# Kernel tuning notes

Hardware: AMD Instinct MI355X
Metric: run time of the kernel (lower is better)

The kernel has to match this reference:

```python
import jax, jax.numpy as jnp
import numpy as np

EMBED_DIM = 1024
HEAD_DIM = 64


def setup_inputs() -> dict:
    key = jax.random.key(0)
    k1, k2, k3, k4 = jax.random.split(key, 4)
    B, T = 4, 4096
    x = jax.random.normal(k1, (B, T, EMBED_DIM), dtype=jnp.float32)
    # nn.Linear(EMBED_DIM, head_dim, bias=False): store as (EMBED_DIM, head_dim)
    s = (1.0 / np.sqrt(EMBED_DIM)).astype(np.float32)
    Wk = jax.random.uniform(k2, (EMBED_DIM, HEAD_DIM), jnp.float32, -s, s)
    Wq = jax.random.uniform(k3, (EMBED_DIM, HEAD_DIM), jnp.float32, -s, s)
    Wv = jax.random.uniform(k4, (EMBED_DIM, HEAD_DIM), jnp.float32, -s, s)
    return {"x": x, "Wq": Wq, "Wk": Wk, "Wv": Wv}


def reference(x, Wq, Wk, Wv):
    B, T, E = x.shape
    q = jnp.einsum('bte,ed->btd', x, Wq)  # (B,T,D)
    k = jnp.einsum('bte,ed->btd', x, Wk)
    v = jnp.einsum('bte,ed->btd', x, Wv)
    # NOTE: original scales by EMBED_DIM**-0.5 (x.size(-1)), not head_dim**-0.5
    scale = jnp.asarray(E, x.dtype) ** -0.5
    scores = jnp.einsum('bqd,bkd->bqk', q, k) * scale  # (B,T,T)
    causal = jnp.tril(jnp.ones((T, T), dtype=bool))
    scores = jnp.where(causal, scores, jnp.asarray(-jnp.inf, scores.dtype))
    attn = jax.nn.softmax(scores, axis=-1)
    # dropout is identity at inference (deterministic baseline)
    out = jnp.einsum('bqk,bkd->bqd', attn, v)  # (B,T,D)
    return out
```

## Files before the change

### kernel.cpp

```cpp
#include <hip/hip_runtime.h>
#include <hip/hip_bf16.h>
#include <stdint.h>

#define BATCH 4
#define SEQ   4096
#define EMB   1024
#define HD    64

typedef __bf16 bf16x8 __attribute__((ext_vector_type(8)));
typedef float  f32x4  __attribute__((ext_vector_type(4)));
typedef unsigned short u16;

union ABFrag { u16 s[8]; bf16x8 v; };

__device__ __forceinline__ u16 f2bf_rne(float f) {
    union { float f; uint32_t u; } cv; cv.f = f;
    uint32_t u = cv.u;
    return (u16)((u + 0x7fffu + ((u >> 16) & 1u)) >> 16);
}
__device__ __forceinline__ float bf2f(u16 h) {
    union { uint32_t u; float f; } cv; cv.u = ((uint32_t)h) << 16;
    return cv.f;
}
__device__ __forceinline__ void gld16(const void* g, void* l) {
    __builtin_amdgcn_global_load_lds(
        (const __attribute__((address_space(1))) void*)g,
        (__attribute__((address_space(3))) void*)l, 16, 0, 0);
}

__global__ __launch_bounds__(256) void wt_kernel(
        const float* __restrict__ Wq, const float* __restrict__ Wk,
        const float* __restrict__ Wv, u16* __restrict__ Wt) {
    int idx = blockIdx.x * 256 + threadIdx.x;
    int i = idx >> 16;
    int r = idx & 65535;
    int n = r >> 10;
    int k = r & 1023;
    const float* W = (i == 0) ? Wq : (i == 1) ? Wk : Wv;
    Wt[idx] = f2bf_rne(W[k * HD + n]);
}

__global__ __launch_bounds__(512) void qkv_kernel(
        const float* __restrict__ x, const u16* __restrict__ Wt,
        u16* __restrict__ Qw, u16* __restrict__ Kw, u16* __restrict__ Vt) {
    __shared__ u16 wl[64 * 1032];

    const int t    = threadIdx.x;
    const int wave = t >> 6;
    const int lane = t & 63;
    const int m16  = lane & 15;
    const int quad = lane >> 4;
    const int wv   = blockIdx.x >> 6;
    const int rb   = blockIdx.x & 63;

    {
        const u16* wsrc = Wt + (wv << 16);
#pragma unroll
        for (int j = 0; j < 16; ++j) {
            const int idx = (wave << 4) + j;
            const int n   = idx >> 1;
            const int hh  = idx & 1;
            gld16(wsrc + (n << 10) + (hh << 9) + (lane << 3),
                  &wl[n * 1032 + (hh << 9)]);
        }
    }
    __syncthreads();

    const int rtA  = (rb << 4) + (wave << 1);
    const int rowA = (rtA << 4) + m16;
    const float* xpA = x + (size_t)rowA * EMB + (quad << 3);
    const float* xpB = xpA + (16 * EMB);

    f32x4 accA[4], accB[4];
#pragma unroll
    for (int tt = 0; tt < 4; ++tt) {
        accA[tt] = (f32x4){0.f, 0.f, 0.f, 0.f};
        accB[tt] = (f32x4){0.f, 0.f, 0.f, 0.f};
    }

    const u16* wbase = &wl[m16 * 1032 + (quad << 3)];

#pragma unroll 2
    for (int kt = 0; kt < 32; ++kt) {
        const float4 a0A = *(const float4*)(xpA + (kt << 5));
        const float4 a1A = *(const float4*)(xpA + (kt << 5) + 4);
        const float4 a0B = *(const float4*)(xpB + (kt << 5));
        const float4 a1B = *(const float4*)(xpB + (kt << 5) + 4);
        ABFrag afA, afB;
        afA.s[0] = f2bf_rne(a0A.x); afA.s[1] = f2bf_rne(a0A.y);
        afA.s[2] = f2bf_rne(a0A.z); afA.s[3] = f2bf_rne(a0A.w);
        afA.s[4] = f2bf_rne(a1A.x); afA.s[5] = f2bf_rne(a1A.y);
        afA.s[6] = f2bf_rne(a1A.z); afA.s[7] = f2bf_rne(a1A.w);
        afB.s[0] = f2bf_rne(a0B.x); afB.s[1] = f2bf_rne(a0B.y);
        afB.s[2] = f2bf_rne(a0B.z); afB.s[3] = f2bf_rne(a0B.w);
        afB.s[4] = f2bf_rne(a1B.x); afB.s[5] = f2bf_rne(a1B.y);
        afB.s[6] = f2bf_rne(a1B.z); afB.s[7] = f2bf_rne(a1B.w);
#pragma unroll
        for (int tt = 0; tt < 4; ++tt) {
            const bf16x8 bf = *(const bf16x8*)(wbase + tt * (16 * 1032) + (kt << 5));
            accA[tt] = __builtin_amdgcn_mfma_f32_16x16x32_bf16(afA.v, bf, accA[tt], 0, 0, 0);
            accB[tt] = __builtin_amdgcn_mfma_f32_16x16x32_bf16(afB.v, bf, accB[tt], 0, 0, 0);
        }
    }

#pragma unroll
    for (int half = 0; half < 2; ++half) {
        const f32x4* acc = half ? accB : accA;
        const int rowbase = ((rtA + half) << 4) + (quad << 2);
        const int bidx = rowbase >> 12;
        const int t0   = rowbase & 4095;
#pragma unroll
        for (int tt = 0; tt < 4; ++tt) {
            const int col = (tt << 4) + m16;
            if (wv == 0) {
#pragma unroll
                for (int reg = 0; reg < 4; ++reg)
                    Qw[(size_t)(rowbase + reg) * HD + col] = f2bf_rne(acc[tt][reg] * 0.03125f);
            } else if (wv == 1) {
#pragma unroll
                for (int reg = 0; reg < 4; ++reg)
                    Kw[(size_t)(rowbase + reg) * HD + col] = f2bf_rne(acc[tt][reg]);
            } else {
                ushort4 vv;
                vv.x = f2bf_rne(acc[tt][0]); vv.y = f2bf_rne(acc[tt][1]);
                vv.z = f2bf_rne(acc[tt][2]); vv.w = f2bf_rne(acc[tt][3]);
                *(ushort4*)(Vt + (size_t)((bidx << 6) + col) * SEQ + t0) = vv;
            }
        }
    }
}

__global__ __launch_bounds__(256) void attn_part_kernel(
        const u16* __restrict__ Qw, const u16* __restrict__ Kw,
        const u16* __restrict__ Vt, u16* __restrict__ Opart,
        float* __restrict__ Mp, float* __restrict__ Lp) {
    __shared__ u16 kv[2][2][4096];
    __shared__ u16 ldsP[4][16 * 72];

    const int pid = blockIdx.x;
    const int r   = pid >> 8;
    const int i   = pid & 255;
    const int b   = i & 3;
    const int h   = i >> 2;
    const int qt  = h ^ (int)((0x1f203f00u >> (r * 8)) & 63u);
    const int c   = r;
    const int p_out = (((b << 6) + qt) << 2) + c;

    const int wave = threadIdx.x >> 6;
    const int lane = threadIdx.x & 63;
    const int m16  = lane & 15;
    const int quad = lane >> 4;

    #define ISSUE_KV(buf_, jt_) do {                                           \
        const int r8_ = lane >> 3, c8_ = lane & 7;                             \
        const int kc_ = c8_ ^ r8_;                                             \
        _Pragma("unroll")                                                      \
        for (int j_ = 0; j_ < 2; ++j_) {                                       \
            const int row_ = ((wave * 2 + j_) << 3) + r8_;          \
            gld16(Kw + ((size_t)(b * SEQ + ((jt_) << 6) + row_) << 6) + (kc_ << 3), \
                  &kv[buf_][0][(wave * 2 + j_) << 9]);                         \
            gld16(Vt + (size_t)((b << 6) + row_) * SEQ + ((jt_) << 6) + (kc_ << 3), \
                  &kv[buf_][1][(wave * 2 + j_) << 9]);                         \
        }                                                                      \
    } while (0)

    const int qrow = (qt << 6) + (wave << 4) + m16;
    const u16* qbase = Qw + ((size_t)(b * SEQ + qrow) << 6);
    const bf16x8 qf0 = *(const bf16x8*)(qbase + (quad << 3));
    const bf16x8 qf1 = *(const bf16x8*)(qbase + 32 + (quad << 3));

    f32x4 acc[4];
#pragma unroll
    for (int dt = 0; dt < 4; ++dt) acc[dt] = (f32x4){0.f, 0.f, 0.f, 0.f};
    float m_i = -3.0e38f;
    float l_i = 0.f;

    u16* ldsW = &ldsP[wave][0];
    const int xs0 = (quad ^ (m16 & 7)) << 3;
    const int xs1 = (((quad + 4)) ^ (m16 & 7)) << 3;

    if (c <= qt) ISSUE_KV(0, c);

    int buf = 0;
    for (int jt = c; jt <= qt; jt += 4) {
        __syncthreads();
        if (jt + 4 <= qt) ISSUE_KV(buf ^ 1, jt + 4);

        f32x4 s[4];
#pragma unroll
        for (int mt = 0; mt < 4; ++mt) {
            const int base = ((mt << 4) + m16) << 6;
            bf16x8 k0 = *(const bf16x8*)&kv[buf][0][base + xs0];
            bf16x8 k1 = *(const bf16x8*)&kv[buf][0][base + xs1];
            s[mt] = (f32x4){0.f, 0.f, 0.f, 0.f};
            s[mt] = __builtin_amdgcn_mfma_f32_16x16x32_bf16(k0, qf0, s[mt], 0, 0, 0);
            s[mt] = __builtin_amdgcn_mfma_f32_16x16x32_bf16(k1, qf1, s[mt], 0, 0, 0);
        }

        if (jt == qt) {
            const int q_in = (wave << 4) + m16;
#pragma unroll
            for (int mt = 0; mt < 4; ++mt) {
                const int k_in = (mt << 4) + (quad << 2);
#pragma unroll
                for (int reg = 0; reg < 4; ++reg)
                    if (k_in + reg > q_in) s[mt][reg] = -3.0e38f;
            }
        }

        float tm = fmaxf(fmaxf(s[0][0], s[0][1]), fmaxf(s[0][2], s[0][3]));
#pragma unroll
        for (int mt = 1; mt < 4; ++mt)
            tm = fmaxf(tm, fmaxf(fmaxf(s[mt][0], s[mt][1]), fmaxf(s[mt][2], s[mt][3])));
        tm = fmaxf(tm, __shfl_xor(tm, 16));
        tm = fmaxf(tm, __shfl_xor(tm, 32));

        const float mnew  = fmaxf(m_i, tm);
        const float alpha = __expf(m_i - mnew);
        m_i = mnew;

        float psum = 0.f;
#pragma unroll
        for (int mt = 0; mt < 4; ++mt) {
            const float p0 = __expf(s[mt][0] - mnew);
            const float p1 = __expf(s[mt][1] - mnew);
            const float p2 = __expf(s[mt][2] - mnew);
            const float p3 = __expf(s[mt][3] - mnew);
            psum += (p0 + p1) + (p2 + p3);
            ushort4 pv;
            pv.x = f2bf_rne(p0); pv.y = f2bf_rne(p1);
            pv.z = f2bf_rne(p2); pv.w = f2bf_rne(p3);
            *(ushort4*)(ldsW + m16 * 72 + (mt << 4) + (quad << 2)) = pv;
        }
        l_i = l_i * alpha + psum;
#pragma unroll
        for (int dt = 0; dt < 4; ++dt)
#pragma unroll
            for (int reg = 0; reg < 4; ++reg) acc[dt][reg] *= alpha;

        const bf16x8 p0 = *(const bf16x8*)(ldsW + m16 * 72 + (quad << 3));
        const bf16x8 p1 = *(const bf16x8*)(ldsW + m16 * 72 + 32 + (quad << 3));
#pragma unroll
        for (int dt = 0; dt < 4; ++dt) {
            const int base = ((dt << 4) + m16) << 6;
            bf16x8 v0 = *(const bf16x8*)&kv[buf][1][base + xs0];
            bf16x8 v1 = *(const bf16x8*)&kv[buf][1][base + xs1];
            acc[dt] = __builtin_amdgcn_mfma_f32_16x16x32_bf16(v0, p0, acc[dt], 0, 0, 0);
            acc[dt] = __builtin_amdgcn_mfma_f32_16x16x32_bf16(v1, p1, acc[dt], 0, 0, 0);
        }
        buf ^= 1;
    }
    #undef ISSUE_KV

    float l = l_i;
    l += __shfl_xor(l, 16);
    l += __shfl_xor(l, 32);

    u16* ob = Opart + (size_t)p_out * 4096;
    const int qin = (wave << 4) + m16;
#pragma unroll
    for (int dt = 0; dt < 4; ++dt) {
        ushort4 vv;
        vv.x = f2bf_rne(acc[dt][0]); vv.y = f2bf_rne(acc[dt][1]);
        vv.z = f2bf_rne(acc[dt][2]); vv.w = f2bf_rne(acc[dt][3]);
        *(ushort4*)(ob + qin * 64 + (dt << 4) + (quad << 2)) = vv;
    }
    if (quad == 0) {
        Mp[p_out * 64 + qin] = m_i;
        Lp[p_out * 64 + qin] = l;
    }
}

__global__ __launch_bounds__(256) void combine_kernel(
        const u16* __restrict__ Opart, const float* __restrict__ Mp,
        const float* __restrict__ Lp, float* __restrict__ out) {
    __shared__ float sm[4][16];
    __shared__ float sl[4][16];
    const int bq = blockIdx.x >> 2;
    const int rq = blockIdx.x & 3;
    const int pidbase = bq << 2;
    const int t = threadIdx.x;
    if (t < 64) {
        const int cc = t >> 4, rr = t & 15;
        sm[cc][rr] = Mp[(pidbase + cc) * 64 + rq * 16 + rr];
        sl[cc][rr] = Lp[(pidbase + cc) * 64 + rq * 16 + rr];
    }
    __syncthreads();

    const int row_l = t >> 4;
    const int c4    = (t & 15) << 2;
    const int row   = rq * 16 + row_l;

    const float M = fmaxf(fmaxf(sm[0][row_l], sm[1][row_l]),
                          fmaxf(sm[2][row_l], sm[3][row_l]));
    float n0 = 0.f, n1 = 0.f, n2 = 0.f, n3 = 0.f, den = 0.f;
#pragma unroll
    for (int cc = 0; cc < 4; ++cc) {
        const float w = __expf(sm[cc][row_l] - M);
        den += w * sl[cc][row_l];
        const ushort4 op = *(const ushort4*)&Opart[
                (size_t)(pidbase + cc) * 4096 + row * 64 + c4];
        n0 += w * bf2f(op.x); n1 += w * bf2f(op.y);
        n2 += w * bf2f(op.z); n3 += w * bf2f(op.w);
    }
    const float rd = 1.0f / den;
    float4 o; o.x = n0 * rd; o.y = n1 * rd; o.z = n2 * rd; o.w = n3 * rd;
    *(float4*)&out[((size_t)bq << 12) + (row << 6) + c4] = o;
}

extern "C" void kernel_launch(void* const* d_in, const int* in_sizes, int n_in,
                              void* d_out, int out_size, void* d_ws, size_t ws_size,
                              hipStream_t stream) {
    const float* x  = (const float*)d_in[0];
    const float* Wq = (const float*)d_in[1];
    const float* Wk = (const float*)d_in[2];
    const float* Wv = (const float*)d_in[3];
    float* out = (float*)d_out;

    char* ws = (char*)d_ws;
    u16* Qw    = (u16*)(ws);
    u16* Kw    = (u16*)(ws + (2u << 20));
    u16* Vt    = (u16*)(ws + (4u << 20));
    u16* Wt    = (u16*)(ws + (6u << 20));
    u16* Opart = (u16*)(ws + (13u << 19));
    float* Mp  = (float*)(ws + (29u << 19));
    float* Lp  = (float*)(ws + (59u << 18));

    wt_kernel<<<768, 256, 0, stream>>>(Wq, Wk, Wv, Wt);
    qkv_kernel<<<192, 512, 0, stream>>>(x, Wt, Qw, Kw, Vt);
    attn_part_kernel<<<1024, 256, 0, stream>>>(Qw, Kw, Vt, Opart, Mp, Lp);
    combine_kernel<<<1024, 256, 0, stream>>>(Opart, Mp, Lp, out);
}
```

Before: 160.1 us.

## Use 128-row query tiles with 8 waves sharing each K/V tile load

The attention kernel now runs 512-thread blocks that each handle 128 query rows (eight waves) instead of 64, so every K/V tile staged in LDS is reused by twice as many waves. The split-K chunk and tile mapping is redone to pair short and long causal rows (i vs 31-i) for load balance. Waves whose rows end earlier skip the last tile. The combine kernel is reindexed to match the new layout. This halves global K/V traffic per query row, at the cost of fewer blocks and some idle waves on the diagonal tile.

```diff
diff --git a/kernel.cpp b/kernel.cpp
--- a/kernel.cpp
+++ b/kernel.cpp
@@ -130,41 +130,41 @@
     }
 }
 
-__global__ __launch_bounds__(256) void attn_part_kernel(
+__global__ __launch_bounds__(512) void attn_part_kernel(
         const u16* __restrict__ Qw, const u16* __restrict__ Kw,
         const u16* __restrict__ Vt, u16* __restrict__ Opart,
         float* __restrict__ Mp, float* __restrict__ Lp) {
     __shared__ u16 kv[2][2][4096];
-    __shared__ u16 ldsP[4][16 * 72];
+    __shared__ u16 ldsP[8][16 * 72];
 
     const int pid = blockIdx.x;
     const int r   = pid >> 8;
-    const int i   = pid & 255;
-    const int b   = i & 3;
-    const int h   = i >> 2;
-    const int qt  = h ^ (int)((0x1f203f00u >> (r * 8)) & 63u);
-    const int c   = r;
-    const int p_out = (((b << 6) + qt) << 2) + c;
+    const int s   = pid & 255;
+    const int b   = s >> 6;
+    const int i0  = (s >> 1) & 31;
+    const int ch  = s & 1;
+    const int i   = r ? (31 - i0) : i0;
+    const int c   = (ch << 1) | r;
+    const int jmax = (i << 1) + 1;
+    const int p_out = (((b << 5) + i) << 2) + c;
 
     const int wave = threadIdx.x >> 6;
     const int lane = threadIdx.x & 63;
     const int m16  = lane & 15;
     const int quad = lane >> 4;
+    const int jend = (i << 1) + (wave >> 2);
 
     #define ISSUE_KV(buf_, jt_) do {                                           \
         const int r8_ = lane >> 3, c8_ = lane & 7;                             \
         const int kc_ = c8_ ^ r8_;                                             \
-        _Pragma("unroll")                                                      \
-        for (int j_ = 0; j_ < 2; ++j_) {                                       \
-            const int row_ = ((wave * 2 + j_) << 3) + r8_;          \
-            gld16(Kw + ((size_t)(b * SEQ + ((jt_) << 6) + row_) << 6) + (kc_ << 3), \
-                  &kv[buf_][0][(wave * 2 + j_) << 9]);                         \
-            gld16(Vt + (size_t)((b << 6) + row_) * SEQ + ((jt_) << 6) + (kc_ << 3), \
-                  &kv[buf_][1][(wave * 2 + j_) << 9]);                         \
-        }                                                                      \
+        const int row_ = (wave << 3) + r8_;                         \
+        gld16(Kw + ((size_t)(b * SEQ + ((jt_) << 6) + row_) << 6) + (kc_ << 3),\
+              &kv[buf_][0][wave << 9]);                                        \
+        gld16(Vt + (size_t)((b << 6) + row_) * SEQ + ((jt_) << 6) + (kc_ << 3),\
+              &kv[buf_][1][wave << 9]);                                        \
     } while (0)
 
-    const int qrow = (qt << 6) + (wave << 4) + m16;
+    const int qrow = (i << 7) + (wave << 4) + m16;
     const u16* qbase = Qw + ((size_t)(b * SEQ + qrow) << 6);
     const bf16x8 qf0 = *(const bf16x8*)(qbase + (quad << 3));
     const bf16x8 qf1 = *(const bf16x8*)(qbase + 32 + (quad << 3));
@@ -177,76 +177,78 @@
 
     u16* ldsW = &ldsP[wave][0];
     const int xs0 = (quad ^ (m16 & 7)) << 3;
-    const int xs1 = (((quad + 4)) ^ (m16 & 7)) << 3;
-
-    if (c <= qt) ISSUE_KV(0, c);
+    const int xs1 = ((quad + 4) ^ (m16 & 7)) << 3;
+
+    if (c <= jmax) ISSUE_KV(0, c);
 
     int buf = 0;
-    for (int jt = c; jt <= qt; jt += 4) {
+    for (int jt = c; jt <= jmax; jt += 4) {
         __syncthreads();
-        if (jt + 4 <= qt) ISSUE_KV(buf ^ 1, jt + 4);
-
-        f32x4 s[4];
-#pragma unroll
-        for (int mt = 0; mt < 4; ++mt) {
-            const int base = ((mt << 4) + m16) << 6;
-            bf16x8 k0 = *(const bf16x8*)&kv[buf][0][base + xs0];
-            bf16x8 k1 = *(const bf16x8*)&kv[buf][0][base + xs1];
-            s[mt] = (f32x4){0.f, 0.f, 0.f, 0.f};
-            s[mt] = __builtin_amdgcn_mfma_f32_16x16x32_bf16(k0, qf0, s[mt], 0, 0, 0);
-            s[mt] = __builtin_amdgcn_mfma_f32_16x16x32_bf16(k1, qf1, s[mt], 0, 0, 0);
-        }
-
-        if (jt == qt) {
-            const int q_in = (wave << 4) + m16;
+        if (jt + 4 <= jmax) ISSUE_KV(buf ^ 1, jt + 4);
+
+        if (jt <= jend) {
+            f32x4 sv[4];
 #pragma unroll
             for (int mt = 0; mt < 4; ++mt) {
-                const int k_in = (mt << 4) + (quad << 2);
-#pragma unroll
-                for (int reg = 0; reg < 4; ++reg)
-                    if (k_in + reg > q_in) s[mt][reg] = -3.0e38f;
-            }
-        }
-
-        float tm = fmaxf(fmaxf(s[0][0], s[0][1]), fmaxf(s[0][2], s[0][3]));
-#pragma unroll
-        for (int mt = 1; mt < 4; ++mt)
-            tm = fmaxf(tm, fmaxf(fmaxf(s[mt][0], s[mt][1]), fmaxf(s[mt][2], s[mt][3])));
-        tm = fmaxf(tm, __shfl_xor(tm, 16));
-        tm = fmaxf(tm, __shfl_xor(tm, 32));
-
-        const float mnew  = fmaxf(m_i, tm);
-        const float alpha = __expf(m_i - mnew);
-        m_i = mnew;
-
-        float psum = 0.f;
-#pragma unroll
-        for (int mt = 0; mt < 4; ++mt) {
-            const float p0 = __expf(s[mt][0] - mnew);
-            const float p1 = __expf(s[mt][1] - mnew);
-            const float p2 = __expf(s[mt][2] - mnew);
-            const float p3 = __expf(s[mt][3] - mnew);
-            psum += (p0 + p1) + (p2 + p3);
-            ushort4 pv;
-            pv.x = f2bf_rne(p0); pv.y = f2bf_rne(p1);
-            pv.z = f2bf_rne(p2); pv.w = f2bf_rne(p3);
-            *(ushort4*)(ldsW + m16 * 72 + (mt << 4) + (quad << 2)) = pv;
-        }
-        l_i = l_i * alpha + psum;
-#pragma unroll
-        for (int dt = 0; dt < 4; ++dt)
-#pragma unroll
-            for (int reg = 0; reg < 4; ++reg) acc[dt][reg] *= alpha;
-
-        const bf16x8 p0 = *(const bf16x8*)(ldsW + m16 * 72 + (quad << 3));
-        const bf16x8 p1 = *(const bf16x8*)(ldsW + m16 * 72 + 32 + (quad << 3));
-#pragma unroll
-        for (int dt = 0; dt < 4; ++dt) {
-            const int base = ((dt << 4) + m16) << 6;
-            bf16x8 v0 = *(const bf16x8*)&kv[buf][1][base + xs0];
-            bf16x8 v1 = *(const bf16x8*)&kv[buf][1][base + xs1];
-            acc[dt] = __builtin_amdgcn_mfma_f32_16x16x32_bf16(v0, p0, acc[dt], 0, 0, 0);
-            acc[dt] = __builtin_amdgcn_mfma_f32_16x16x32_bf16(v1, p1, acc[dt], 0, 0, 0);
+                const int base = ((mt << 4) + m16) << 6;
+                bf16x8 k0 = *(const bf16x8*)&kv[buf][0][base + xs0];
+                bf16x8 k1 = *(const bf16x8*)&kv[buf][0][base + xs1];
+                sv[mt] = (f32x4){0.f, 0.f, 0.f, 0.f};
+                sv[mt] = __builtin_amdgcn_mfma_f32_16x16x32_bf16(k0, qf0, sv[mt], 0, 0, 0);
+                sv[mt] = __builtin_amdgcn_mfma_f32_16x16x32_bf16(k1, qf1, sv[mt], 0, 0, 0);
+            }
+
+            if (jt == jend) {
+                const int q_in = ((wave & 3) << 4) + m16;
+#pragma unroll
+                for (int mt = 0; mt < 4; ++mt) {
+                    const int k_in = (mt << 4) + (quad << 2);
+#pragma unroll
+                    for (int reg = 0; reg < 4; ++reg)
+                        if (k_in + reg > q_in) sv[mt][reg] = -3.0e38f;
+                }
+            }
+
+            float tm = fmaxf(fmaxf(sv[0][0], sv[0][1]), fmaxf(sv[0][2], sv[0][3]));
+#pragma unroll
+            for (int mt = 1; mt < 4; ++mt)
+                tm = fmaxf(tm, fmaxf(fmaxf(sv[mt][0], sv[mt][1]), fmaxf(sv[mt][2], sv[mt][3])));
+            tm = fmaxf(tm, __shfl_xor(tm, 16));
+            tm = fmaxf(tm, __shfl_xor(tm, 32));
+
+            const float mnew  = fmaxf(m_i, tm);
+            const float alpha = __expf(m_i - mnew);
+            m_i = mnew;
+
+            float psum = 0.f;
+#pragma unroll
+            for (int mt = 0; mt < 4; ++mt) {
+                const float p0 = __expf(sv[mt][0] - mnew);
+                const float p1 = __expf(sv[mt][1] - mnew);
+                const float p2 = __expf(sv[mt][2] - mnew);
+                const float p3 = __expf(sv[mt][3] - mnew);
+                psum += (p0 + p1) + (p2 + p3);
+                ushort4 pv;
+                pv.x = f2bf_rne(p0); pv.y = f2bf_rne(p1);
+                pv.z = f2bf_rne(p2); pv.w = f2bf_rne(p3);
+                *(ushort4*)(ldsW + m16 * 72 + (mt << 4) + (quad << 2)) = pv;
+            }
+            l_i = l_i * alpha + psum;
+#pragma unroll
+            for (int dt = 0; dt < 4; ++dt)
+#pragma unroll
+                for (int reg = 0; reg < 4; ++reg) acc[dt][reg] *= alpha;
+
+            const bf16x8 p0 = *(const bf16x8*)(ldsW + m16 * 72 + (quad << 3));
+            const bf16x8 p1 = *(const bf16x8*)(ldsW + m16 * 72 + 32 + (quad << 3));
+#pragma unroll
+            for (int dt = 0; dt < 4; ++dt) {
+                const int base = ((dt << 4) + m16) << 6;
+                bf16x8 v0 = *(const bf16x8*)&kv[buf][1][base + xs0];
+                bf16x8 v1 = *(const bf16x8*)&kv[buf][1][base + xs1];
+                acc[dt] = __builtin_amdgcn_mfma_f32_16x16x32_bf16(v0, p0, acc[dt], 0, 0, 0);
+                acc[dt] = __builtin_amdgcn_mfma_f32_16x16x32_bf16(v1, p1, acc[dt], 0, 0, 0);
+            }
         }
         buf ^= 1;
     }
@@ -256,7 +258,7 @@
     l += __shfl_xor(l, 16);
     l += __shfl_xor(l, 32);
 
-    u16* ob = Opart + (size_t)p_out * 4096;
+    u16* ob = Opart + ((size_t)p_out << 13);
     const int qin = (wave << 4) + m16;
 #pragma unroll
     for (int dt = 0; dt < 4; ++dt) {
@@ -266,8 +268,8 @@
         *(ushort4*)(ob + qin * 64 + (dt << 4) + (quad << 2)) = vv;
     }
     if (quad == 0) {
-        Mp[p_out * 64 + qin] = m_i;
-        Lp[p_out * 64 + qin] = l;
+        Mp[(p_out << 7) + qin] = m_i;
+        Lp[(p_out << 7) + qin] = l;
     }
 }
 
@@ -276,20 +278,20 @@
         const float* __restrict__ Lp, float* __restrict__ out) {
     __shared__ float sm[4][16];
     __shared__ float sl[4][16];
-    const int bq = blockIdx.x >> 2;
-    const int rq = blockIdx.x & 3;
-    const int pidbase = bq << 2;
+    const int bi = blockIdx.x >> 3;
+    const int rq = blockIdx.x & 7;
+    const int pidbase = bi << 2;
     const int t = threadIdx.x;
     if (t < 64) {
         const int cc = t >> 4, rr = t & 15;
-        sm[cc][rr] = Mp[(pidbase + cc) * 64 + rq * 16 + rr];
-        sl[cc][rr] = Lp[(pidbase + cc) * 64 + rq * 16 + rr];
+        sm[cc][rr] = Mp[((pidbase + cc) << 7) + (rq << 4) + rr];
+        sl[cc][rr] = Lp[((pidbase + cc) << 7) + (rq << 4) + rr];
     }
     __syncthreads();
 
     const int row_l = t >> 4;
     const int c4    = (t & 15) << 2;
-    const int row   = rq * 16 + row_l;
+    const int row   = (rq << 4) + row_l;
 
     const float M = fmaxf(fmaxf(sm[0][row_l], sm[1][row_l]),
                           fmaxf(sm[2][row_l], sm[3][row_l]));
@@ -299,13 +301,14 @@
         const float w = __expf(sm[cc][row_l] - M);
         den += w * sl[cc][row_l];
         const ushort4 op = *(const ushort4*)&Opart[
-                (size_t)(pidbase + cc) * 4096 + row * 64 + c4];
+                ((size_t)(pidbase + cc) << 13) + row * 64 + c4];
         n0 += w * bf2f(op.x); n1 += w * bf2f(op.y);
         n2 += w * bf2f(op.z); n3 += w * bf2f(op.w);
     }
     const float rd = 1.0f / den;
     float4 o; o.x = n0 * rd; o.y = n1 * rd; o.z = n2 * rd; o.w = n3 * rd;
-    *(float4*)&out[((size_t)bq << 12) + (row << 6) + c4] = o;
+    const int brow = (bi >> 5) * SEQ + ((bi & 31) << 7) + row;
+    *(float4*)&out[((size_t)brow << 6) + c4] = o;
 }
 
 extern "C" void kernel_launch(void* const* d_in, const int* in_sizes, int n_in,
@@ -328,6 +331,6 @@
 
     wt_kernel<<<768, 256, 0, stream>>>(Wq, Wk, Wv, Wt);
     qkv_kernel<<<192, 512, 0, stream>>>(x, Wt, Qw, Kw, Vt);
-    attn_part_kernel<<<1024, 256, 0, stream>>>(Qw, Kw, Vt, Opart, Mp, Lp);
+    attn_part_kernel<<<512, 512, 0, stream>>>(Qw, Kw, Vt, Opart, Mp, Lp);
     combine_kernel<<<1024, 256, 0, stream>>>(Opart, Mp, Lp, out);
 }
```

Measured after the change: 153.9 us. -3.9%, faster.
